# Optimization experiments

Measured on AMD Instinct MI355X. Metric: run time of the kernel, lower is better.

## Reference

```python
import jax, jax.numpy as jnp
import numpy as np

D_MODEL = 512
KERNEL = 16
DILATIONS = (1, 1, 2, 2, 4, 4, 8, 8)
HEADS = len(DILATIONS)
HEAD_W = D_MODEL // HEADS
B, L = 2, 1024
MODE = "forward"  # causal: window sees only prior words


def setup_inputs() -> dict:
    key = jax.random.key(0)
    ks = jax.random.split(key, 8)
    s = 0.02  # small init like nn.Linear
    return {
        "tensor": jax.random.normal(ks[0], (B, L, D_MODEL), jnp.float32),
        "Wq": jax.random.normal(ks[1], (HEADS, HEAD_W, D_MODEL), jnp.float32) * s,
        "bq": jnp.zeros((HEADS, HEAD_W), jnp.float32),
        "Wk": jax.random.normal(ks[2], (HEADS, KERNEL, HEAD_W, D_MODEL), jnp.float32) * s,
        "bk": jnp.zeros((HEADS, KERNEL, HEAD_W), jnp.float32),
        "Wv": jax.random.normal(ks[3], (HEADS, KERNEL, HEAD_W, D_MODEL), jnp.float32) * s,
        "bv": jnp.zeros((HEADS, KERNEL, HEAD_W), jnp.float32),
        "Wo": jax.random.normal(ks[4], (D_MODEL, HEADS, HEAD_W), jnp.float32) * s,
        "bo": jnp.zeros((D_MODEL,), jnp.float32),
    }


def _window_indices():
    """Static gather indices replicating Glimpses.dilocal's dilated unfold.

    Returns idx of shape (H, L, K) indexing into a sequence zero-padded by
    max_off on both sides: content[h, l, k] = x_padded[idx[h, l, k]].
    """
    dil = np.asarray(DILATIONS)  # (H,)
    max_off = int((KERNEL - 1) * dil.max())
    if MODE == "forward":
        front = (KERNEL - 1) * dil           # all padding in front (causal)
    elif MODE == "backward":
        front = np.zeros_like(dil)           # all padding behind
    else:  # center
        front = ((KERNEL - 1) * dil) // 2
    l = np.arange(L)[None, :, None]
    k = np.arange(KERNEL)[None, None, :]
    d = dil[:, None, None]
    f = front[:, None, None]
    idx = l + k * d - f + max_off            # (H, L, K), always in-range
    return jnp.asarray(idx), max_off


_IDX, _MOFF = _window_indices()


def reference(tensor, Wq, bq, Wk, bk, Wv, bv, Wo, bo):
    # tensor: (B, L, D)
    xp = jnp.pad(tensor, ((0, 0), (_MOFF, _MOFF), (0, 0)))
    content = xp[:, _IDX, :]                                   # (B,H,L,K,D)
    # per-head query projection (kernel position 1)
    q = jnp.einsum('bld,hod->bhlo', tensor, Wq) + bq[:, None, :]        # (B,H,L,hw)
    # per-(head, kernel-position) independent key/value projections
    k = jnp.einsum('bhlkd,hkod->bhlko', content, Wk) + bk[:, None, :, :]
    v = jnp.einsum('bhlkd,hkod->bhlko', content, Wv) + bv[:, None, :, :]
    # tiny local attention over the K window positions
    logits = jnp.einsum('bhlo,bhlko->bhlk', q, k)               # (B,H,L,K)
    score = jax.nn.softmax(logits, axis=-1)
    # NOTE: original scales AFTER the score@value matmul (faithful to source)
    attn = jnp.einsum('bhlk,bhlko->bhlo', score, v)
    attn = attn / jnp.sqrt(jnp.asarray(HEAD_W, tensor.dtype))   # (B,H,L,hw)
    # dehead: merge (heads, head_width) -> d_model
    out = jnp.einsum('bhlo,dho->bld', attn, Wo) + bo            # (B,L,D)
    return out
```

## Files before the change

kernel.cpp:

```cpp
#include <hip/hip_runtime.h>


#define BD 2
#define LL 1024
#define DM 512
#define HH 8
#define KT 16
#define HW 64

#define NQKV 16896

typedef unsigned short u16;
typedef unsigned int u32;
typedef __bf16 bf16x8 __attribute__((ext_vector_type(8)));
typedef float f32x4 __attribute__((ext_vector_type(4)));
typedef unsigned short ushort4v __attribute__((ext_vector_type(4)));
typedef unsigned short ushort8v __attribute__((ext_vector_type(8)));

__constant__ int c_dil[8] = {1, 1, 2, 2, 4, 4, 8, 8};

__device__ __forceinline__ float bf2f(u16 u) {
    return __builtin_bit_cast(float, (u32)u << 16);
}
__device__ __forceinline__ u16 f2bf(float f) {
    u32 u = __builtin_bit_cast(u32, f);
    return (u16)((u + 0x7fffu + ((u >> 16) & 1u)) >> 16);
}

__device__ __forceinline__ void gl_lds16(const u16* g, u16* l) {
    __builtin_amdgcn_global_load_lds(
        (__attribute__((address_space(1))) void*)g,
        (__attribute__((address_space(3))) void*)l, 16, 0, 0);
}

__global__ __launch_bounds__(256, 4) void gemm_bf16(
    const u16* __restrict__ A, const u16* __restrict__ Bm,
    const float* __restrict__ bq, const float* __restrict__ bk,
    const float* __restrict__ bv, u16* __restrict__ C)
{
    const int m0 = blockIdx.y << 7;
    const int n0 = blockIdx.x << 7;
    if (n0 >= NQKV) return;

    __shared__ u16 As[128 * 32];
    __shared__ u16 Bs[128 * 32];

    const int tid  = threadIdx.x;
    const int wave = tid >> 6, lane = tid & 63;
    const int r0 = tid >> 2;
    const int cc = (tid & 3) << 3;
    const int mw = (wave >> 1) << 6;
    const int nw = (wave & 1) << 6;
    const int lr = lane & 15;
    const int qg = lane >> 4;
    const int ksw = ((qg ^ ((lr >> 1) & 3)) << 3);

    const u16* Ag = A  + (size_t)(m0 + r0) * DM + cc;
    const u16* Bg = Bm + (size_t)(n0 + r0) * DM + cc;
    u16* lA = &As[0] + tid * 8;
    u16* lB = &Bs[0] + tid * 8;

    f32x4 acc[4][4];
#pragma unroll
    for (int i = 0; i < 4; ++i)
#pragma unroll
        for (int j = 0; j < 4; ++j) acc[i][j] = (f32x4){0.f, 0.f, 0.f, 0.f};

    for (int k0 = 0; k0 < DM; k0 += 32) {
        gl_lds16(Ag + k0, lA);
        gl_lds16(Ag + k0 + (size_t)64 * DM, lA + 64 * 32);
        gl_lds16(Bg + k0, lB);
        gl_lds16(Bg + k0 + (size_t)64 * DM, lB + 64 * 32);
        __syncthreads();

        bf16x8 af[4], bfr[4];
#pragma unroll
        for (int i = 0; i < 4; ++i)
            af[i] = *(const bf16x8*)&As[(mw + (i << 4) + lr) * 32 + ksw];
#pragma unroll
        for (int j = 0; j < 4; ++j)
            bfr[j] = *(const bf16x8*)&Bs[(nw + (j << 4) + lr) * 32 + ksw];
#pragma unroll
        for (int i = 0; i < 4; ++i)
#pragma unroll
            for (int j = 0; j < 4; ++j)
                acc[i][j] = __builtin_amdgcn_mfma_f32_16x16x32_bf16(
                    af[i], bfr[j], acc[i][j], 0, 0, 0);
        __syncthreads();
    }

    const float* bias; int cb;
    if      (n0 <  512) { bias = bq; cb = 0;    }
    else if (n0 < 8704) { bias = bk; cb = 512;  }
    else                { bias = bv; cb = 8704; }

#pragma unroll
    for (int i = 0; i < 4; ++i) {
        const int rowb = m0 + mw + (i << 4) + (qg << 2);
#pragma unroll
        for (int j = 0; j < 4; ++j) {
            const int col = n0 + nw + (j << 4) + lr;
            const float bs = bias[col - cb];
#pragma unroll
            for (int r = 0; r < 4; ++r)
                C[(size_t)(rowb + r) * NQKV + col] = f2bf(acc[i][j][r] + bs);
        }
    }
}

__global__ __launch_bounds__(256, 4) void gemm_out(
    const u16* __restrict__ A, const u16* __restrict__ Bm,
    const float* __restrict__ bias, float* __restrict__ C)
{
    __shared__ u16 As[64 * 32];
    __shared__ u16 Bs[64 * 32];

    const int tid  = threadIdx.x;
    const int wave = tid >> 6, lane = tid & 63;
    const int m0 = blockIdx.y << 6, n0 = blockIdx.x << 6;
    const int r0 = tid >> 2, cc = (tid & 3) << 3;
    const int mw = wave << 4;
    const int lr = lane & 15, qg = lane >> 4;
    const int ksw = ((qg ^ ((lr >> 1) & 3)) << 3);

    const u16* Ag = A  + (size_t)(m0 + r0) * DM + cc;
    const u16* Bg = Bm + (size_t)(n0 + r0) * DM + cc;
    u16* lA = &As[0] + tid * 8;
    u16* lB = &Bs[0] + tid * 8;

    f32x4 acc[4];
#pragma unroll
    for (int j = 0; j < 4; ++j) acc[j] = (f32x4){0.f, 0.f, 0.f, 0.f};

    for (int k0 = 0; k0 < DM; k0 += 32) {
        gl_lds16(Ag + k0, lA);
        gl_lds16(Bg + k0, lB);
        __syncthreads();
        bf16x8 af = *(const bf16x8*)&As[(mw + lr) * 32 + ksw];
#pragma unroll
        for (int j = 0; j < 4; ++j) {
            bf16x8 bfr = *(const bf16x8*)&Bs[((j << 4) + lr) * 32 + ksw];
            acc[j] = __builtin_amdgcn_mfma_f32_16x16x32_bf16(af, bfr, acc[j], 0, 0, 0);
        }
        __syncthreads();
    }

#pragma unroll
    for (int j = 0; j < 4; ++j) {
        const int col = n0 + (j << 4) + lr;
        const float bs = bias[col];
#pragma unroll
        for (int r = 0; r < 4; ++r)
            C[(size_t)(m0 + mw + (qg << 2) + r) * DM + col] = acc[j][r] + bs;
    }
}

__global__ void cvt_swz(const float* __restrict__ x,  const float* __restrict__ Wq,
                        const float* __restrict__ Wk, const float* __restrict__ Wv,
                        const float* __restrict__ Wo,
                        u16* __restrict__ xb, u16* __restrict__ wb,
                        u16* __restrict__ wob)
{
    const int i = blockIdx.x * 256 + threadIdx.x;
    const float* src; u16* dst; int t;
    if (i < 131072) {
        t = i;
        src = x;  dst = xb;
    } else if (i < 1212416) {
        t = i - 131072;
        const int row = t >> 6;
        if      (row <  512) src = Wq;
        else if (row < 8704) src = Wk - (size_t)512 * DM;
        else                 src = Wv - (size_t)8704 * DM;
        dst = wb;
    } else {
        t = i - 1212416;
        src = Wo; dst = wob;
    }
    const int row = t >> 6;
    const int c8  = t & 63;
    const int s   = (row >> 1) & 3;
    const int oc  = (c8 & ~3) | ((c8 & 3) ^ s);
    const float* p = src + (size_t)row * DM + (oc << 3);
    float4 v0 = *(const float4*)p;
    float4 v1 = *(const float4*)(p + 4);
    ushort8v o = { f2bf(v0.x), f2bf(v0.y), f2bf(v0.z), f2bf(v0.w),
                   f2bf(v1.x), f2bf(v1.y), f2bf(v1.z), f2bf(v1.w) };
    *(ushort8v*)(dst + (size_t)row * DM + (c8 << 3)) = o;
}

__global__ __launch_bounds__(256, 4) void attn_bf16(
    const u16* __restrict__ qkv,
    const float* __restrict__ bk,
    const float* __restrict__ bv,
    u16* __restrict__ attnb)
{
    const int tid = threadIdx.x;
    const int j  = tid & 7;
    const int ll = tid >> 3;
    const int bid = blockIdx.x;
    const int h = bid & 7;
    const int t = (bid >> 3) & 31;
    const int b = bid >> 8;
    const int l = (t << 5) + ll;
    const int dil = c_dil[h];

    const int hko = h * (KT * HW);
    const size_t rowbase = (size_t)(b * LL) * NQKV + hko + (j << 3);

    float qf[8];
    {
        ushort8v qv = *(const ushort8v*)(qkv + (size_t)(b * LL + l) * NQKV
                                         + h * HW + (j << 3));
#pragma unroll
        for (int z = 0; z < 8; ++z) qf[z] = bf2f(qv[z]);
    }

    ushort8v kr[KT];
#pragma unroll
    for (int k = 0; k < KT; ++k) {
        const int src = l - (KT - 1 - k) * dil;
        if (src >= 0)
            kr[k] = *(const ushort8v*)(qkv + rowbase + (size_t)src * NQKV
                                       + 512 + k * HW);
    }

    float lg[KT];
#pragma unroll
    for (int k = 0; k < KT; ++k) {
        const int src = l - (KT - 1 - k) * dil;
        float p = 0.f;
        if (src >= 0) {
#pragma unroll
            for (int z = 0; z < 8; ++z) p += qf[z] * bf2f(kr[k][z]);
        } else {
            const float* bkp = bk + hko + k * HW + (j << 3);
#pragma unroll
            for (int z = 0; z < 8; ++z) p += qf[z] * bkp[z];
        }
        p += __shfl_xor(p, 1);
        p += __shfl_xor(p, 2);
        p += __shfl_xor(p, 4);
        lg[k] = p;
    }

    float m = lg[0];
#pragma unroll
    for (int k = 1; k < KT; ++k) m = fmaxf(m, lg[k]);
    float s = 0.f;
#pragma unroll
    for (int k = 0; k < KT; ++k) { lg[k] = __expf(lg[k] - m); s += lg[k]; }
    const float inv = 1.f / s;

    ushort8v vr[KT];
#pragma unroll
    for (int k = 0; k < KT; ++k) {
        const int src = l - (KT - 1 - k) * dil;
        if (src >= 0)
            vr[k] = *(const ushort8v*)(qkv + rowbase + (size_t)src * NQKV
                                       + 8704 + k * HW);
    }

    float acc[8];
#pragma unroll
    for (int z = 0; z < 8; ++z) acc[z] = 0.f;
#pragma unroll
    for (int k = 0; k < KT; ++k) {
        const int src = l - (KT - 1 - k) * dil;
        const float sc = lg[k] * inv;
        if (src >= 0) {
#pragma unroll
            for (int z = 0; z < 8; ++z) acc[z] = fmaf(sc, bf2f(vr[k][z]), acc[z]);
        } else {
            const float* bvp = bv + hko + k * HW + (j << 3);
#pragma unroll
            for (int z = 0; z < 8; ++z) acc[z] = fmaf(sc, bvp[z], acc[z]);
        }
    }

    ushort8v o;
#pragma unroll
    for (int z = 0; z < 8; ++z) o[z] = f2bf(acc[z] * 0.125f);
    const int row = b * LL + l;
    const int k8 = h * 8 + j;
    const int sw = ((k8 & 3) ^ ((l >> 1) & 3)) << 3;
    *(ushort8v*)(attnb + (size_t)row * DM + ((k8 >> 2) << 5) + sw) = o;
}

__global__ __launch_bounds__(256, 2) void gemm_nt_bias(
    const float* __restrict__ A, const float* __restrict__ Bm,
    const float* __restrict__ bias, float* __restrict__ C,
    int M, int N, int Kd)
{
    __shared__ float As[16][68];
    __shared__ float Bs[16][68];
    const int tid = threadIdx.x;
    const int tx = tid & 15, ty = tid >> 4;
    const int r0 = blockIdx.y << 6, c0 = blockIdx.x << 6;
    const int lr = tid >> 2, k4 = (tid & 3) << 2;
    const float* Ap = A  + (size_t)(r0 + lr) * Kd + k4;
    const float* Bp = Bm + (size_t)(c0 + lr) * Kd + k4;
    float acc[4][4];
#pragma unroll
    for (int i = 0; i < 4; ++i)
#pragma unroll
        for (int j = 0; j < 4; ++j) acc[i][j] = 0.f;
    for (int d0 = 0; d0 < Kd; d0 += 16) {
        float4 av = *(const float4*)(Ap + d0);
        float4 bv = *(const float4*)(Bp + d0);
        As[k4 + 0][lr] = av.x; As[k4 + 1][lr] = av.y;
        As[k4 + 2][lr] = av.z; As[k4 + 3][lr] = av.w;
        Bs[k4 + 0][lr] = bv.x; Bs[k4 + 1][lr] = bv.y;
        Bs[k4 + 2][lr] = bv.z; Bs[k4 + 3][lr] = bv.w;
        __syncthreads();
#pragma unroll
        for (int dd = 0; dd < 16; ++dd) {
            float4 a4 = *(const float4*)&As[dd][ty << 2];
            float4 b4 = *(const float4*)&Bs[dd][tx << 2];
            float ar[4] = {a4.x, a4.y, a4.z, a4.w};
            float br[4] = {b4.x, b4.y, b4.z, b4.w};
#pragma unroll
            for (int i = 0; i < 4; ++i)
#pragma unroll
                for (int j = 0; j < 4; ++j)
                    acc[i][j] = fmaf(ar[i], br[j], acc[i][j]);
        }
        __syncthreads();
    }
#pragma unroll
    for (int i = 0; i < 4; ++i) {
        float4 o;
        const int c = c0 + (tx << 2);
        o.x = acc[i][0] + bias[c + 0];
        o.y = acc[i][1] + bias[c + 1];
        o.z = acc[i][2] + bias[c + 2];
        o.w = acc[i][3] + bias[c + 3];
        *(float4*)&C[(size_t)(r0 + (ty << 2) + i) * N + c] = o;
    }
}

__device__ __forceinline__ void tile_gemm_f32(
    const float* __restrict__ xb, int src, bool ok,
    const float* __restrict__ wrow,
    int lr, int k4, int tx, int ty,
    float (&As)[16][68], float (&Ws)[16][68], float (&acc)[4][4])
{
#pragma unroll
    for (int i = 0; i < 4; ++i)
#pragma unroll
        for (int j = 0; j < 4; ++j) acc[i][j] = 0.f;
    const float* xrow = xb + (size_t)(ok ? src : 0) * DM + k4;
    for (int d0 = 0; d0 < DM; d0 += 16) {
        float4 av = make_float4(0.f, 0.f, 0.f, 0.f);
        if (ok) av = *(const float4*)(xrow + d0);
        float4 wv = *(const float4*)(wrow + d0);
        As[k4 + 0][lr] = av.x; As[k4 + 1][lr] = av.y;
        As[k4 + 2][lr] = av.z; As[k4 + 3][lr] = av.w;
        Ws[k4 + 0][lr] = wv.x; Ws[k4 + 1][lr] = wv.y;
        Ws[k4 + 2][lr] = wv.z; Ws[k4 + 3][lr] = wv.w;
        __syncthreads();
#pragma unroll
        for (int dd = 0; dd < 16; ++dd) {
            float4 a4 = *(const float4*)&As[dd][ty << 2];
            float4 b4 = *(const float4*)&Ws[dd][tx << 2];
            float ar[4] = {a4.x, a4.y, a4.z, a4.w};
            float br[4] = {b4.x, b4.y, b4.z, b4.w};
#pragma unroll
            for (int i = 0; i < 4; ++i)
#pragma unroll
                for (int j = 0; j < 4; ++j)
                    acc[i][j] = fmaf(ar[i], br[j], acc[i][j]);
        }
        __syncthreads();
    }
}

__global__ __launch_bounds__(256, 2) void attn_kernel(
    const float* __restrict__ x, const float* __restrict__ q,
    const float* __restrict__ Wk, const float* __restrict__ bk,
    const float* __restrict__ Wv, const float* __restrict__ bv,
    float* __restrict__ attn)
{
    __shared__ float As[16][68];
    __shared__ float Ws[16][68];
    __shared__ float qs[64][68];
    __shared__ float lg[64][17];
    __shared__ float red[64][17];
    const int tid = threadIdx.x;
    const int tx = tid & 15, ty = tid >> 4;
    const int bid = blockIdx.x;
    const int h = bid & 7, t = (bid >> 3) & 15, b = bid >> 7;
    const int l0 = t << 6;
    const int dil = c_dil[h];
    const int lr = tid >> 2, k4 = (tid & 3) << 2;
    for (int i = tid; i < 64 * 16; i += 256) {
        int l = i >> 4, o4 = (i & 15) << 2;
        float4 v = *(const float4*)&q[((size_t)(b * LL + l0 + l) * HH + h) * HW + o4];
        *(float4*)&qs[l][o4] = v;
    }
    const float* xb  = x  + (size_t)b * LL * DM;
    const float* Wkh = Wk + (size_t)h * KT * HW * DM;
    const float* Wvh = Wv + (size_t)h * KT * HW * DM;
    const float* bkh = bk + h * KT * HW;
    const float* bvh = bv + h * KT * HW;
    float acc[4][4];
    for (int kk = 0; kk < KT; ++kk) {
        const int src = l0 + lr - (KT - 1 - kk) * dil;
        const bool ok = (src >= 0) && (src < LL);
        tile_gemm_f32(xb, src, ok, Wkh + (size_t)(kk * HW + lr) * DM + k4,
                      lr, k4, tx, ty, As, Ws, acc);
        const float* bkp = bkh + kk * HW + (tx << 2);
#pragma unroll
        for (int i = 0; i < 4; ++i) {
            float p = 0.f;
#pragma unroll
            for (int j = 0; j < 4; ++j)
                p += (acc[i][j] + bkp[j]) * qs[(ty << 2) + i][(tx << 2) + j];
            red[(ty << 2) + i][tx] = p;
        }
        __syncthreads();
        if (tid < 64) {
            float s = 0.f;
#pragma unroll
            for (int u = 0; u < 16; ++u) s += red[tid][u];
            lg[tid][kk] = s;
        }
        __syncthreads();
    }
    if (tid < 64) {
        float m = lg[tid][0];
#pragma unroll
        for (int u = 1; u < KT; ++u) m = fmaxf(m, lg[tid][u]);
        float s = 0.f;
#pragma unroll
        for (int u = 0; u < KT; ++u) {
            float e = expf(lg[tid][u] - m);
            lg[tid][u] = e; s += e;
        }
        float inv = 1.f / s;
#pragma unroll
        for (int u = 0; u < KT; ++u) lg[tid][u] *= inv;
    }
    __syncthreads();
    float vacc[4][4];
#pragma unroll
    for (int i = 0; i < 4; ++i)
#pragma unroll
        for (int j = 0; j < 4; ++j) vacc[i][j] = 0.f;
    for (int kk = 0; kk < KT; ++kk) {
        const int src = l0 + lr - (KT - 1 - kk) * dil;
        const bool ok = (src >= 0) && (src < LL);
        tile_gemm_f32(xb, src, ok, Wvh + (size_t)(kk * HW + lr) * DM + k4,
                      lr, k4, tx, ty, As, Ws, acc);
        const float* bvp = bvh + kk * HW + (tx << 2);
#pragma unroll
        for (int i = 0; i < 4; ++i) {
            float sc = lg[(ty << 2) + i][kk];
#pragma unroll
            for (int j = 0; j < 4; ++j)
                vacc[i][j] = fmaf(sc, acc[i][j] + bvp[j], vacc[i][j]);
        }
    }
#pragma unroll
    for (int i = 0; i < 4; ++i) {
        float4 o;
        o.x = vacc[i][0] * 0.125f;
        o.y = vacc[i][1] * 0.125f;
        o.z = vacc[i][2] * 0.125f;
        o.w = vacc[i][3] * 0.125f;
        *(float4*)&attn[((size_t)(b * LL + l0 + (ty << 2) + i) * HH + h) * HW + (tx << 2)] = o;
    }
}

extern "C" void kernel_launch(void* const* d_in, const int* in_sizes, int n_in,
                              void* d_out, int out_size, void* d_ws, size_t ws_size,
                              hipStream_t stream)
{
    const float* x  = (const float*)d_in[0];
    const float* Wq = (const float*)d_in[1];
    const float* bq = (const float*)d_in[2];
    const float* Wk = (const float*)d_in[3];
    const float* bk = (const float*)d_in[4];
    const float* Wv = (const float*)d_in[5];
    const float* bv = (const float*)d_in[6];
    const float* Wo = (const float*)d_in[7];
    const float* bo = (const float*)d_in[8];
    float* out = (float*)d_out;

    const int M = BD * LL;

    const size_t N_X   = (size_t)BD * LL * DM;
    const size_t N_WB  = (size_t)NQKV * DM;
    const size_t N_WO  = (size_t)DM * DM;
    const size_t N_QKV = (size_t)M * NQKV;
    const size_t NEED  = (N_X + N_WB + N_WO + N_QKV + N_X) * 2;

    if (ws_size >= NEED) {
        u16* xb    = (u16*)d_ws;
        u16* wb    = xb    + N_X;
        u16* wob   = wb    + N_WB;
        u16* qkv   = wob   + N_WO;
        u16* attnb = qkv   + N_QKV;

        cvt_swz<<<4864, 256, 0, stream>>>(x, Wq, Wk, Wv, Wo, xb, wb, wob);

        gemm_bf16<<<dim3(136, 16), 256, 0, stream>>>(
            xb, wb, bq, bk, bv, qkv);

        attn_bf16<<<BD * HH * (LL / 32), 256, 0, stream>>>(
            qkv, bk, bv, attnb);

        gemm_out<<<dim3(8, 32), 256, 0, stream>>>(attnb, wob, bo, out);
    } else {
        float* qws = (float*)d_ws;
        float* aws = qws + (size_t)BD * LL * HH * HW;
        gemm_nt_bias<<<dim3((HH * HW) / 64, M / 64), 256, 0, stream>>>(
            x, Wq, bq, qws, M, HH * HW, DM);
        attn_kernel<<<BD * HH * (LL / 64), 256, 0, stream>>>(
            x, qws, Wk, bk, Wv, bv, aws);
        gemm_nt_bias<<<dim3(DM / 64, M / 64), 256, 0, stream>>>(
            aws, Wo, bo, out, M, DM, HH * HW);
    }
}
```

Before: 168.4 us.

## Double-buffer QKV GEMM with 128x256 tiles, 512 threads, and XCD-aware block remap

```diff
diff --git a/kernel.cpp b/kernel.cpp
--- a/kernel.cpp
+++ b/kernel.cpp
@@ -33,32 +33,38 @@
         (__attribute__((address_space(3))) void*)l, 16, 0, 0);
 }
 
-__global__ __launch_bounds__(256, 4) void gemm_bf16(
+__device__ __forceinline__ void bar() {
+    asm volatile("" ::: "memory");
+    __builtin_amdgcn_s_barrier();
+    asm volatile("" ::: "memory");
+}
+
+__global__ __launch_bounds__(512, 2) void gemm_bf16(
     const u16* __restrict__ A, const u16* __restrict__ Bm,
     const float* __restrict__ bq, const float* __restrict__ bk,
     const float* __restrict__ bv, u16* __restrict__ C)
 {
-    const int m0 = blockIdx.y << 7;
-    const int n0 = blockIdx.x << 7;
-    if (n0 >= NQKV) return;
-
-    __shared__ u16 As[128 * 32];
-    __shared__ u16 Bs[128 * 32];
+    __shared__ u16 As[2][2][128 * 32];
+    __shared__ u16 Bs[2][2][256 * 32];
+
+    const int bid = blockIdx.x;
+    const int wg  = (bid & 7) * 132 + (bid >> 3);
+    const int m0  = (wg & 15) << 7;
+    const int n0  = (wg >> 4) << 8;
 
     const int tid  = threadIdx.x;
-    const int wave = tid >> 6, lane = tid & 63;
+    const int wid  = tid >> 6, lane = tid & 63;
+    const int wm   = wid >> 2;
+    const int wn   = wid & 3;
+    const int lr   = lane & 15, qg = lane >> 4;
+    const int ksw  = ((qg ^ ((lr >> 1) & 3)) << 3);
+
     const int r0 = tid >> 2;
-    const int cc = (tid & 3) << 3;
-    const int mw = (wave >> 1) << 6;
-    const int nw = (wave & 1) << 6;
-    const int lr = lane & 15;
-    const int qg = lane >> 4;
-    const int ksw = ((qg ^ ((lr >> 1) & 3)) << 3);
-
-    const u16* Ag = A  + (size_t)(m0 + r0) * DM + cc;
-    const u16* Bg = Bm + (size_t)(n0 + r0) * DM + cc;
-    u16* lA = &As[0] + tid * 8;
-    u16* lB = &Bs[0] + tid * 8;
+    const int c8 = (tid & 3) << 3;
+    const u16* Ag = A  + (size_t)(m0 + r0) * DM + c8;
+    const u16* Bg = Bm + (size_t)(n0 + r0) * DM + c8;
+    u16* lA = &As[0][0][0] + tid * 8;
+    u16* lB = &Bs[0][0][0] + tid * 8;
 
     f32x4 acc[4][4];
 #pragma unroll
@@ -66,28 +72,50 @@
 #pragma unroll
         for (int j = 0; j < 4; ++j) acc[i][j] = (f32x4){0.f, 0.f, 0.f, 0.f};
 
-    for (int k0 = 0; k0 < DM; k0 += 32) {
-        gl_lds16(Ag + k0, lA);
-        gl_lds16(Ag + k0 + (size_t)64 * DM, lA + 64 * 32);
-        gl_lds16(Bg + k0, lB);
-        gl_lds16(Bg + k0 + (size_t)64 * DM, lB + 64 * 32);
-        __syncthreads();
-
-        bf16x8 af[4], bfr[4];
-#pragma unroll
-        for (int i = 0; i < 4; ++i)
-            af[i] = *(const bf16x8*)&As[(mw + (i << 4) + lr) * 32 + ksw];
-#pragma unroll
-        for (int j = 0; j < 4; ++j)
-            bfr[j] = *(const bf16x8*)&Bs[(nw + (j << 4) + lr) * 32 + ksw];
-#pragma unroll
-        for (int i = 0; i < 4; ++i)
-#pragma unroll
-            for (int j = 0; j < 4; ++j)
-                acc[i][j] = __builtin_amdgcn_mfma_f32_16x16x32_bf16(
-                    af[i], bfr[j], acc[i][j], 0, 0, 0);
-        __syncthreads();
-    }
+#define STAGE(t2, ks, c) do {                                              \
+        const int ko_ = ((t2) << 6) + ((ks) << 5);                         \
+        gl_lds16(Ag + ko_, lA + ((c) * 2 + (ks)) * 4096);                  \
+        gl_lds16(Bg + ko_, lB + ((c) * 2 + (ks)) * 8192);                  \
+        gl_lds16(Bg + ko_ + (size_t)128 * DM,                              \
+                 lB + ((c) * 2 + (ks)) * 8192 + 4096);                     \
+    } while (0)
+
+    STAGE(0, 0, 0); STAGE(0, 1, 0);
+    STAGE(1, 0, 1); STAGE(1, 1, 1);
+    asm volatile("s_waitcnt vmcnt(6)" ::: "memory");
+    bar();
+
+#pragma unroll
+    for (int t = 0; t < 8; ++t) {
+        const int c = t & 1;
+#pragma unroll
+        for (int ks = 0; ks < 2; ++ks) {
+            bf16x8 af[4], bfr[4];
+#pragma unroll
+            for (int m = 0; m < 4; ++m)
+                af[m] = *(const bf16x8*)
+                    &As[c][ks][((wm << 6) + (m << 4) + lr) * 32 + ksw];
+#pragma unroll
+            for (int n = 0; n < 4; ++n)
+                bfr[n] = *(const bf16x8*)
+                    &Bs[c][ks][((wn << 6) + (n << 4) + lr) * 32 + ksw];
+            asm volatile("s_waitcnt lgkmcnt(0)" ::: "memory");
+            bar();
+            if (t < 6) STAGE(t + 2, ks, c);
+            __builtin_amdgcn_s_setprio(1);
+#pragma unroll
+            for (int m = 0; m < 4; ++m)
+#pragma unroll
+                for (int n = 0; n < 4; ++n)
+                    acc[m][n] = __builtin_amdgcn_mfma_f32_16x16x32_bf16(
+                        af[m], bfr[n], acc[m][n], 0, 0, 0);
+            __builtin_amdgcn_s_setprio(0);
+        }
+        if (t < 6)       asm volatile("s_waitcnt vmcnt(6)" ::: "memory");
+        else if (t == 6) asm volatile("s_waitcnt vmcnt(0)" ::: "memory");
+        bar();
+    }
+#undef STAGE
 
     const float* bias; int cb;
     if      (n0 <  512) { bias = bq; cb = 0;    }
@@ -95,15 +123,15 @@
     else                { bias = bv; cb = 8704; }
 
 #pragma unroll
-    for (int i = 0; i < 4; ++i) {
-        const int rowb = m0 + mw + (i << 4) + (qg << 2);
-#pragma unroll
-        for (int j = 0; j < 4; ++j) {
-            const int col = n0 + nw + (j << 4) + lr;
+    for (int m = 0; m < 4; ++m) {
+        const int rowb = m0 + (wm << 6) + (m << 4) + (qg << 2);
+#pragma unroll
+        for (int n = 0; n < 4; ++n) {
+            const int col = n0 + (wn << 6) + (n << 4) + lr;
             const float bs = bias[col - cb];
 #pragma unroll
             for (int r = 0; r < 4; ++r)
-                C[(size_t)(rowb + r) * NQKV + col] = f2bf(acc[i][j][r] + bs);
+                C[(size_t)(rowb + r) * NQKV + col] = f2bf(acc[m][n][r] + bs);
         }
     }
 }
@@ -504,7 +532,7 @@
 
         cvt_swz<<<4864, 256, 0, stream>>>(x, Wq, Wk, Wv, Wo, xb, wb, wob);
 
-        gemm_bf16<<<dim3(136, 16), 256, 0, stream>>>(
+        gemm_bf16<<<dim3(1056), 512, 0, stream>>>(
             xb, wb, bq, bk, bv, qkv);
 
         attn_bf16<<<BD * HH * (LL / 32), 256, 0, stream>>>(
```

After: 181.3 us. 7.6% more time.
